# Performance work log

Measured on AMD Instinct MI355X. Metric: run time of the kernel, lower is better.

The kernel has to match this reference:

```python
import jax, jax.numpy as jnp
from jax import lax
import numpy as np

WINDOW = 51
HALF = WINDOW // 2  # 25
K_SAUVOLA = 0.2     # skimage threshold_sauvola default k
RGB_W = np.array([0.2989, 0.5870, 0.1140], dtype=np.float32)  # tf.image.rgb_to_grayscale weights


def _window_sum(x, axis):
    """Sliding-window sum of length WINDOW along `axis`, 'same' size, reflect padding.
    O(1) per pixel via cumulative sums (integral-image style), matching the
    uniform_filter-based local statistics in skimage's Sauvola."""
    pad = [(0, 0)] * x.ndim
    pad[axis] = (HALF, HALF)
    xp = jnp.pad(x, pad, mode='reflect')
    cs = jnp.cumsum(xp, axis=axis)
    zshape = list(cs.shape)
    zshape[axis] = 1
    cs = jnp.concatenate([jnp.zeros(zshape, cs.dtype), cs], axis=axis)
    n = cs.shape[axis]
    hi = lax.slice_in_dim(cs, WINDOW, n, axis=axis)
    lo = lax.slice_in_dim(cs, 0, n - WINDOW, axis=axis)
    return hi - lo


def _box_mean(x):
    # separable 51x51 box filter over H (axis 1) and W (axis 2)
    s = _window_sum(_window_sum(x, axis=1), axis=2)
    return s / jnp.asarray(WINDOW * WINDOW, x.dtype)


def setup_inputs() -> dict:
    key = jax.random.key(0)
    inputs = jax.random.uniform(key, (8, 1024, 1024, 3), dtype=jnp.float32)
    return {"inputs": inputs}


def reference(inputs) -> jnp.ndarray:
    # RGB -> grayscale (channels == 3 branch), keep channel dim [B,H,W,1]
    gray = jnp.einsum('bhwc,c->bhw', inputs, jnp.asarray(RGB_W))[..., None]
    # local mean / std over 51x51 window
    m = _box_mean(gray)
    m2 = _box_mean(gray * gray)
    var = jnp.maximum(m2 - m * m, 0.0)
    s = jnp.sqrt(var)
    # skimage default dynamic range: r = 0.5 * (max - min) over the whole array
    r = 0.5 * (jnp.max(gray) - jnp.min(gray))
    thresh = m * (1.0 + K_SAUVOLA * (s / r - 1.0))
    # (gray > thresh) * 1
    return (gray > thresh).astype(jnp.float32)
```

## Files before the change

### kernel.cpp

```cpp
#include <hip/hip_runtime.h>

#define IMW 1024
#define IMH 1024
#define NB  8
#define HALF 25
#define STRIP 64
#define NCELL 64

#define W_R ((double)0.2989f)
#define W_G ((double)0.5870f)
#define W_B ((double)0.1140f)
#define INV_AREA (1.0 / 2601.0)

__device__ __forceinline__ int refl(int i, int n) {
    if (i < 0) i = -i;
    if (i >= n) i = 2 * n - 2 - i;
    return i;
}

__device__ __forceinline__ double wsum(const double* __restrict__ C, int p) {
    int a = p + HALF; if (a > IMW - 1) a = IMW - 1;
    int b = p - HALF - 1;
    double s = C[a] - (b >= 0 ? C[b] : 0.0);
    if (p <= HALF - 1)      s += C[HALF - p] - C[0];
    if (p >= IMW - HALF)    s += C[IMW - 2] - C[2*IMW - 2 - HALF - 1 - p];
    return s;
}

__global__ void k0_init(unsigned long long* cells) {
    cells[threadIdx.x] = ~0ULL;
    cells[NCELL + threadIdx.x] = 0ULL;
}

__global__ __launch_bounds__(256) void k1_rowpass(const float* __restrict__ in,
                                                  double2* __restrict__ hp,
                                                  unsigned long long* __restrict__ cells) {
    __shared__ double cs1[IMW];
    __shared__ double cs2[IMW];
    __shared__ double wt1[4], wt2[4], bmin[4], bmax[4];
    const int row = blockIdx.x;
    const long long base = (long long)row * IMW;
    const int t = threadIdx.x;
    const int lane = t & 63, w = t >> 6;

    const float4* p4 = (const float4*)(in + base * 3);
    float4 f0 = p4[3*t], f1 = p4[3*t+1], f2 = p4[3*t+2];
    double g0 = (double)f0.x*W_R + (double)f0.y*W_G + (double)f0.z*W_B;
    double g1 = (double)f0.w*W_R + (double)f1.x*W_G + (double)f1.y*W_B;
    double g2 = (double)f1.z*W_R + (double)f1.w*W_G + (double)f2.x*W_B;
    double g3 = (double)f2.y*W_R + (double)f2.z*W_G + (double)f2.w*W_B;

    double l1_0 = g0, l1_1 = l1_0 + g1, l1_2 = l1_1 + g2, l1_3 = l1_2 + g3;
    double q0 = g0*g0, q1 = g1*g1, q2 = g2*g2, q3 = g3*g3;
    double l2_0 = q0, l2_1 = l2_0 + q1, l2_2 = l2_1 + q2, l2_3 = l2_2 + q3;

    double lmin = fmin(fmin(g0, g1), fmin(g2, g3));
    double lmax = fmax(fmax(g0, g1), fmax(g2, g3));
    for (int off = 32; off; off >>= 1) {
        lmin = fmin(lmin, __shfl_down(lmin, off));
        lmax = fmax(lmax, __shfl_down(lmax, off));
    }
    if (lane == 0) { bmin[w] = lmin; bmax[w] = lmax; }

    double v1 = l1_3, v2 = l2_3;
    for (int off = 1; off < 64; off <<= 1) {
        double u1 = __shfl_up(v1, off);
        double u2 = __shfl_up(v2, off);
        if (lane >= off) { v1 += u1; v2 += u2; }
    }
    if (lane == 63) { wt1[w] = v1; wt2[w] = v2; }
    __syncthreads();
    double e1 = v1 - l1_3, e2 = v2 - l2_3;
    for (int j = 0; j < w; j++) { e1 += wt1[j]; e2 += wt2[j]; }

    double2* c1 = (double2*)&cs1[4*t];
    double2* c2 = (double2*)&cs2[4*t];
    c1[0] = make_double2(e1 + l1_0, e1 + l1_1);
    c1[1] = make_double2(e1 + l1_2, e1 + l1_3);
    c2[0] = make_double2(e2 + l2_0, e2 + l2_1);
    c2[1] = make_double2(e2 + l2_2, e2 + l2_3);

    if (t == 0) {
        double m0 = fmin(fmin(bmin[0], bmin[1]), fmin(bmin[2], bmin[3]));
        double m1 = fmax(fmax(bmax[0], bmax[1]), fmax(bmax[2], bmax[3]));
        int cell = row & (NCELL - 1);
        atomicMin(&cells[cell], (unsigned long long)__double_as_longlong(m0));
        atomicMax(&cells[NCELL + cell], (unsigned long long)__double_as_longlong(m1));
    }
    __syncthreads();

    for (int k = 0; k < 4; k++) {
        int p = t + 256 * k;
        hp[base + p] = make_double2(wsum(cs1, p), wsum(cs2, p));
    }
}

__global__ __launch_bounds__(256) void k2_colpass(const float* __restrict__ in,
                                                  const double2* __restrict__ hp,
                                                  const unsigned long long* __restrict__ cells,
                                                  float* __restrict__ out) {
    __shared__ double sr[2];
    const int t = threadIdx.x;
    if (t < 64) {
        unsigned long long mn = cells[t];
        unsigned long long mx = cells[NCELL + t];
        for (int off = 32; off; off >>= 1) {
            unsigned long long a = __shfl_down(mn, off);
            unsigned long long b = __shfl_down(mx, off);
            mn = (a < mn) ? a : mn;
            mx = (b > mx) ? b : mx;
        }
        if (t == 0) {
            sr[0] = __longlong_as_double((long long)mn);
            sr[1] = __longlong_as_double((long long)mx);
        }
    }
    __syncthreads();
    const double r  = 0.5 * (sr[1] - sr[0]);
    const double r2 = r * r;

    const int id   = blockIdx.x;
    const int b    = id & 7;
    const int rest = id >> 3;
    const int ys   = rest & 15;
    const int xc   = rest >> 4;
    const int x  = xc * 256 + t;
    const int y0 = ys * STRIP;
    const long long ib = (long long)b * IMH * IMW;

    double2 v = make_double2(0.0, 0.0);
    #pragma unroll 8
    for (int j = -HALF; j <= HALF; j++) {
        int ry = refl(y0 + j, IMH);
        double2 h = hp[ib + (long long)ry * IMW + x];
        v.x += h.x; v.y += h.y;
    }

    #pragma unroll 8
    for (int y = y0; y < y0 + STRIP; y++) {
        long long pix = ib + (long long)y * IMW + x;
        const float* p = in + pix * 3;
        double g = (double)p[0]*W_R + (double)p[1]*W_G + (double)p[2]*W_B;

        double m  = v.x * INV_AREA;
        double va = fmax(v.y * INV_AREA - m * m, 0.0);
        double A  = g - 0.8 * m;
        int o = (A > 0.0) && (A * A * r2 > 0.04 * m * m * va);
        out[pix] = o ? 1.0f : 0.0f;

        int ra = refl(y + HALF + 1, IMH);
        int rs = refl(y - HALF, IMH);
        double2 ha = hp[ib + (long long)ra * IMW + x];
        double2 hs = hp[ib + (long long)rs * IMW + x];
        v.x += ha.x - hs.x;
        v.y += ha.y - hs.y;
    }
}

extern "C" void kernel_launch(void* const* d_in, const int* in_sizes, int n_in,
                              void* d_out, int out_size, void* d_ws, size_t ws_size,
                              hipStream_t stream) {
    const float* in = (const float*)d_in[0];
    float* out = (float*)d_out;

    unsigned long long* cells = (unsigned long long*)d_ws;
    double2* hp = (double2*)((char*)d_ws + 4096);

    hipLaunchKernelGGL(k0_init, dim3(1), dim3(NCELL), 0, stream, cells);
    hipLaunchKernelGGL(k1_rowpass, dim3(NB * IMH), dim3(256), 0, stream,
                       in, hp, cells);
    hipLaunchKernelGGL(k2_colpass, dim3((IMW / 256) * (IMH / STRIP) * NB), dim3(256), 0, stream,
                       in, hp, cells, out);
}
```

Before: 237.6 us.

## Replace sliding column sum with slab-wise vertical prefix sums plus carry

The row pass now handles 8-row slabs per block and writes running vertical prefix sums of the horizontal window sums within each slab. A new carry kernel computes per-slab column offsets. The column pass then gets each window sum in O(1) from prefix differences, so it no longer needs a 51-row warmup, and it uses shorter strips for more parallelism. In exchange it adds an extra kernel launch and more random-ish hp reads per pixel (about 4 double2 loads instead of 2), and prefix sums in double may lose some precision.

```diff
diff --git a/kernel.cpp b/kernel.cpp
--- a/kernel.cpp
+++ b/kernel.cpp
@@ -4,19 +4,15 @@
 #define IMH 1024
 #define NB  8
 #define HALF 25
-#define STRIP 64
+#define SLAB 8
+#define NSLAB (IMH / SLAB)
+#define STRIP 16
 #define NCELL 64
 
 #define W_R ((double)0.2989f)
 #define W_G ((double)0.5870f)
 #define W_B ((double)0.1140f)
 #define INV_AREA (1.0 / 2601.0)
-
-__device__ __forceinline__ int refl(int i, int n) {
-    if (i < 0) i = -i;
-    if (i >= n) i = 2 * n - 2 - i;
-    return i;
-}
 
 __device__ __forceinline__ double wsum(const double* __restrict__ C, int p) {
     int a = p + HALF; if (a > IMW - 1) a = IMW - 1;
@@ -32,73 +28,106 @@
     cells[NCELL + threadIdx.x] = 0ULL;
 }
 
-__global__ __launch_bounds__(256) void k1_rowpass(const float* __restrict__ in,
-                                                  double2* __restrict__ hp,
-                                                  unsigned long long* __restrict__ cells) {
+__global__ __launch_bounds__(256) void k1_slab(const float* __restrict__ in,
+                                               double2* __restrict__ hp,
+                                               unsigned long long* __restrict__ cells) {
     __shared__ double cs1[IMW];
     __shared__ double cs2[IMW];
-    __shared__ double wt1[4], wt2[4], bmin[4], bmax[4];
-    const int row = blockIdx.x;
-    const long long base = (long long)row * IMW;
+    __shared__ double wt1[4], wt2[4];
+    const int blk = blockIdx.x;
+    const int b = blk / NSLAB;
+    const int s = blk % NSLAB;
+    const int r0 = s * SLAB;
     const int t = threadIdx.x;
     const int lane = t & 63, w = t >> 6;
 
-    const float4* p4 = (const float4*)(in + base * 3);
-    float4 f0 = p4[3*t], f1 = p4[3*t+1], f2 = p4[3*t+2];
-    double g0 = (double)f0.x*W_R + (double)f0.y*W_G + (double)f0.z*W_B;
-    double g1 = (double)f0.w*W_R + (double)f1.x*W_G + (double)f1.y*W_B;
-    double g2 = (double)f1.z*W_R + (double)f1.w*W_G + (double)f2.x*W_B;
-    double g3 = (double)f2.y*W_R + (double)f2.z*W_G + (double)f2.w*W_B;
-
-    double l1_0 = g0, l1_1 = l1_0 + g1, l1_2 = l1_1 + g2, l1_3 = l1_2 + g3;
-    double q0 = g0*g0, q1 = g1*g1, q2 = g2*g2, q3 = g3*g3;
-    double l2_0 = q0, l2_1 = l2_0 + q1, l2_2 = l2_1 + q2, l2_3 = l2_2 + q3;
-
-    double lmin = fmin(fmin(g0, g1), fmin(g2, g3));
-    double lmax = fmax(fmax(g0, g1), fmax(g2, g3));
+    double acc1[4] = {0.0, 0.0, 0.0, 0.0};
+    double acc2[4] = {0.0, 0.0, 0.0, 0.0};
+    double lmin = 1e300, lmax = -1e300;
+
+    for (int r = 0; r < SLAB; r++) {
+        const int row = r0 + r;
+        const long long base = ((long long)b * IMH + row) * IMW;
+
+        const float4* p4 = (const float4*)(in + base * 3);
+        float4 f0 = p4[3*t], f1 = p4[3*t+1], f2 = p4[3*t+2];
+        double g0 = (double)f0.x*W_R + (double)f0.y*W_G + (double)f0.z*W_B;
+        double g1 = (double)f0.w*W_R + (double)f1.x*W_G + (double)f1.y*W_B;
+        double g2 = (double)f1.z*W_R + (double)f1.w*W_G + (double)f2.x*W_B;
+        double g3 = (double)f2.y*W_R + (double)f2.z*W_G + (double)f2.w*W_B;
+
+        double l1_0 = g0, l1_1 = l1_0 + g1, l1_2 = l1_1 + g2, l1_3 = l1_2 + g3;
+        double q0 = g0*g0, q1 = g1*g1, q2 = g2*g2, q3 = g3*g3;
+        double l2_0 = q0, l2_1 = l2_0 + q1, l2_2 = l2_1 + q2, l2_3 = l2_2 + q3;
+
+        lmin = fmin(lmin, fmin(fmin(g0, g1), fmin(g2, g3)));
+        lmax = fmax(lmax, fmax(fmax(g0, g1), fmax(g2, g3)));
+
+        double v1 = l1_3, v2 = l2_3;
+        for (int off = 1; off < 64; off <<= 1) {
+            double u1 = __shfl_up(v1, off);
+            double u2 = __shfl_up(v2, off);
+            if (lane >= off) { v1 += u1; v2 += u2; }
+        }
+        __syncthreads();
+        if (lane == 63) { wt1[w] = v1; wt2[w] = v2; }
+        __syncthreads();
+        double e1 = v1 - l1_3, e2 = v2 - l2_3;
+        for (int j = 0; j < w; j++) { e1 += wt1[j]; e2 += wt2[j]; }
+
+        double2* c1 = (double2*)&cs1[4*t];
+        double2* c2 = (double2*)&cs2[4*t];
+        c1[0] = make_double2(e1 + l1_0, e1 + l1_1);
+        c1[1] = make_double2(e1 + l1_2, e1 + l1_3);
+        c2[0] = make_double2(e2 + l2_0, e2 + l2_1);
+        c2[1] = make_double2(e2 + l2_2, e2 + l2_3);
+        __syncthreads();
+
+        #pragma unroll
+        for (int k = 0; k < 4; k++) {
+            int p = t + 256 * k;
+            acc1[k] += wsum(cs1, p);
+            acc2[k] += wsum(cs2, p);
+            hp[base + p] = make_double2(acc1[k], acc2[k]);
+        }
+    }
+
     for (int off = 32; off; off >>= 1) {
         lmin = fmin(lmin, __shfl_down(lmin, off));
         lmax = fmax(lmax, __shfl_down(lmax, off));
     }
+    __shared__ double bmin[4], bmax[4];
     if (lane == 0) { bmin[w] = lmin; bmax[w] = lmax; }
-
-    double v1 = l1_3, v2 = l2_3;
-    for (int off = 1; off < 64; off <<= 1) {
-        double u1 = __shfl_up(v1, off);
-        double u2 = __shfl_up(v2, off);
-        if (lane >= off) { v1 += u1; v2 += u2; }
-    }
-    if (lane == 63) { wt1[w] = v1; wt2[w] = v2; }
     __syncthreads();
-    double e1 = v1 - l1_3, e2 = v2 - l2_3;
-    for (int j = 0; j < w; j++) { e1 += wt1[j]; e2 += wt2[j]; }
-
-    double2* c1 = (double2*)&cs1[4*t];
-    double2* c2 = (double2*)&cs2[4*t];
-    c1[0] = make_double2(e1 + l1_0, e1 + l1_1);
-    c1[1] = make_double2(e1 + l1_2, e1 + l1_3);
-    c2[0] = make_double2(e2 + l2_0, e2 + l2_1);
-    c2[1] = make_double2(e2 + l2_2, e2 + l2_3);
-
     if (t == 0) {
         double m0 = fmin(fmin(bmin[0], bmin[1]), fmin(bmin[2], bmin[3]));
         double m1 = fmax(fmax(bmax[0], bmax[1]), fmax(bmax[2], bmax[3]));
-        int cell = row & (NCELL - 1);
+        int cell = blk & (NCELL - 1);
         atomicMin(&cells[cell], (unsigned long long)__double_as_longlong(m0));
         atomicMax(&cells[NCELL + cell], (unsigned long long)__double_as_longlong(m1));
     }
-    __syncthreads();
-
-    for (int k = 0; k < 4; k++) {
-        int p = t + 256 * k;
-        hp[base + p] = make_double2(wsum(cs1, p), wsum(cs2, p));
-    }
-}
-
-__global__ __launch_bounds__(256) void k2_colpass(const float* __restrict__ in,
-                                                  const double2* __restrict__ hp,
-                                                  const unsigned long long* __restrict__ cells,
-                                                  float* __restrict__ out) {
+}
+
+__global__ __launch_bounds__(256) void k1c_carry(const double2* __restrict__ hp,
+                                                 double2* __restrict__ carry) {
+    const int tid = blockIdx.x * 256 + threadIdx.x;
+    const int b = tid >> 10;
+    const int col = tid & (IMW - 1);
+    double a1 = 0.0, a2 = 0.0;
+    #pragma unroll 8
+    for (int s = 0; s < NSLAB; s++) {
+        carry[((long long)b * NSLAB + s) * IMW + col] = make_double2(a1, a2);
+        double2 v = hp[((long long)b * IMH + s * SLAB + SLAB - 1) * IMW + col];
+        a1 += v.x;
+        a2 += v.y;
+    }
+}
+
+__global__ __launch_bounds__(256) void k2_cpass(const float* __restrict__ in,
+                                                const double2* __restrict__ hp,
+                                                const double2* __restrict__ carry,
+                                                const unsigned long long* __restrict__ cells,
+                                                float* __restrict__ out) {
     __shared__ double sr[2];
     const int t = threadIdx.x;
     if (t < 64) {
@@ -106,9 +135,9 @@
         unsigned long long mx = cells[NCELL + t];
         for (int off = 32; off; off >>= 1) {
             unsigned long long a = __shfl_down(mn, off);
-            unsigned long long b = __shfl_down(mx, off);
+            unsigned long long b2 = __shfl_down(mx, off);
             mn = (a < mn) ? a : mn;
-            mx = (b > mx) ? b : mx;
+            mx = (b2 > mx) ? b2 : mx;
         }
         if (t == 0) {
             sr[0] = __longlong_as_double((long long)mn);
@@ -122,38 +151,57 @@
     const int id   = blockIdx.x;
     const int b    = id & 7;
     const int rest = id >> 3;
-    const int ys   = rest & 15;
-    const int xc   = rest >> 4;
-    const int x  = xc * 256 + t;
+    const int ys   = rest & 63;
+    const int xt   = rest >> 6;
+    const int x  = xt * 256 + t;
     const int y0 = ys * STRIP;
     const long long ib = (long long)b * IMH * IMW;
-
-    double2 v = make_double2(0.0, 0.0);
-    #pragma unroll 8
-    for (int j = -HALF; j <= HALF; j++) {
-        int ry = refl(y0 + j, IMH);
-        double2 h = hp[ib + (long long)ry * IMW + x];
-        v.x += h.x; v.y += h.y;
-    }
-
-    #pragma unroll 8
+    const double2* Cb = hp + ib;
+    const double2* Kb = carry + (long long)b * NSLAB * IMW;
+
+    #pragma unroll 2
     for (int y = y0; y < y0 + STRIP; y++) {
+        const int top = (y + HALF > IMH - 1) ? (IMH - 1) : (y + HALF);
+        const int bot = y - HALF - 1;
+
+        double2 ct = Cb[(long long)top * IMW + x];
+        double2 kt = Kb[(long long)(top >> 3) * IMW + x];
+        double V1 = ct.x + kt.x;
+        double V2 = ct.y + kt.y;
+        if (bot >= 0) {
+            double2 cbv = Cb[(long long)bot * IMW + x];
+            double2 kbv = Kb[(long long)(bot >> 3) * IMW + x];
+            V1 -= cbv.x + kbv.x;
+            V2 -= cbv.y + kbv.y;
+        }
+        if (y <= HALF - 1) {
+            int ma = HALF - y;
+            double2 c1 = Cb[(long long)ma * IMW + x];
+            double2 k1 = Kb[(long long)(ma >> 3) * IMW + x];
+            double2 c0 = Cb[x];
+            double2 k0 = Kb[x];
+            V1 += (c1.x + k1.x) - (c0.x + k0.x);
+            V2 += (c1.y + k1.y) - (c0.y + k0.y);
+        }
+        if (y + HALF > IMH - 1) {
+            int mz = 2 * IMH - 4 - HALF - y + 1;
+            double2 c1 = Cb[(long long)(IMH - 2) * IMW + x];
+            double2 k1 = Kb[(long long)((IMH - 2) >> 3) * IMW + x];
+            double2 c0 = Cb[(long long)mz * IMW + x];
+            double2 k0 = Kb[(long long)(mz >> 3) * IMW + x];
+            V1 += (c1.x + k1.x) - (c0.x + k0.x);
+            V2 += (c1.y + k1.y) - (c0.y + k0.y);
+        }
+
         long long pix = ib + (long long)y * IMW + x;
         const float* p = in + pix * 3;
         double g = (double)p[0]*W_R + (double)p[1]*W_G + (double)p[2]*W_B;
 
-        double m  = v.x * INV_AREA;
-        double va = fmax(v.y * INV_AREA - m * m, 0.0);
+        double m  = V1 * INV_AREA;
+        double va = fmax(V2 * INV_AREA - m * m, 0.0);
         double A  = g - 0.8 * m;
         int o = (A > 0.0) && (A * A * r2 > 0.04 * m * m * va);
         out[pix] = o ? 1.0f : 0.0f;
-
-        int ra = refl(y + HALF + 1, IMH);
-        int rs = refl(y - HALF, IMH);
-        double2 ha = hp[ib + (long long)ra * IMW + x];
-        double2 hs = hp[ib + (long long)rs * IMW + x];
-        v.x += ha.x - hs.x;
-        v.y += ha.y - hs.y;
     }
 }
 
@@ -165,10 +213,13 @@
 
     unsigned long long* cells = (unsigned long long*)d_ws;
     double2* hp = (double2*)((char*)d_ws + 4096);
+    double2* carry = hp + (size_t)NB * IMH * IMW;
 
     hipLaunchKernelGGL(k0_init, dim3(1), dim3(NCELL), 0, stream, cells);
-    hipLaunchKernelGGL(k1_rowpass, dim3(NB * IMH), dim3(256), 0, stream,
+    hipLaunchKernelGGL(k1_slab, dim3(NB * NSLAB), dim3(256), 0, stream,
                        in, hp, cells);
-    hipLaunchKernelGGL(k2_colpass, dim3((IMW / 256) * (IMH / STRIP) * NB), dim3(256), 0, stream,
-                       in, hp, cells, out);
-}
+    hipLaunchKernelGGL(k1c_carry, dim3(NB * IMW / 256), dim3(256), 0, stream,
+                       hp, carry);
+    hipLaunchKernelGGL(k2_cpass, dim3((IMW / 256) * (IMH / STRIP) * NB), dim3(256), 0, stream,
+                       in, hp, carry, cells, out);
+}
```

After: 272.2 us. +14.6%, slower.

## Add per-slab column partial sums to shortcut column-window initialization

Applied to the files above, without the earlier changes.

The row pass now processes 8-row slabs per block and, besides the horizontal window sums, writes per-slab column sums of those values. The column pass initializes its 51-row vertical window from these slab sums plus a few edge rows instead of reading all 51 rows, and it skips the unused final slide. This reduces global reads in the column pass, at the cost of an extra workspace buffer and fewer, longer row-pass blocks with more barriers.

```diff
diff --git a/kernel.cpp b/kernel.cpp
--- a/kernel.cpp
+++ b/kernel.cpp
@@ -4,7 +4,10 @@
 #define IMH 1024
 #define NB  8
 #define HALF 25
+#define SLAB 8
+#define NSLAB (IMH / SLAB)
 #define STRIP 64
+#define NSTRIP (IMH / STRIP)
 #define NCELL 64
 
 #define W_R ((double)0.2989f)
@@ -32,71 +35,117 @@
     cells[NCELL + threadIdx.x] = 0ULL;
 }
 
-__global__ __launch_bounds__(256) void k1_rowpass(const float* __restrict__ in,
-                                                  double2* __restrict__ hp,
-                                                  unsigned long long* __restrict__ cells) {
+__global__ __launch_bounds__(256) void k1_slab(const float* __restrict__ in,
+                                               double2* __restrict__ hp,
+                                               double2* __restrict__ Sv,
+                                               unsigned long long* __restrict__ cells) {
     __shared__ double cs1[IMW];
     __shared__ double cs2[IMW];
-    __shared__ double wt1[4], wt2[4], bmin[4], bmax[4];
-    const int row = blockIdx.x;
-    const long long base = (long long)row * IMW;
+    __shared__ double wt1[4], wt2[4];
+    const int blk = blockIdx.x;
+    const int b = blk / NSLAB;
+    const int s = blk % NSLAB;
+    const int r0 = s * SLAB;
     const int t = threadIdx.x;
     const int lane = t & 63, w = t >> 6;
 
-    const float4* p4 = (const float4*)(in + base * 3);
-    float4 f0 = p4[3*t], f1 = p4[3*t+1], f2 = p4[3*t+2];
-    double g0 = (double)f0.x*W_R + (double)f0.y*W_G + (double)f0.z*W_B;
-    double g1 = (double)f0.w*W_R + (double)f1.x*W_G + (double)f1.y*W_B;
-    double g2 = (double)f1.z*W_R + (double)f1.w*W_G + (double)f2.x*W_B;
-    double g3 = (double)f2.y*W_R + (double)f2.z*W_G + (double)f2.w*W_B;
-
-    double l1_0 = g0, l1_1 = l1_0 + g1, l1_2 = l1_1 + g2, l1_3 = l1_2 + g3;
-    double q0 = g0*g0, q1 = g1*g1, q2 = g2*g2, q3 = g3*g3;
-    double l2_0 = q0, l2_1 = l2_0 + q1, l2_2 = l2_1 + q2, l2_3 = l2_2 + q3;
-
-    double lmin = fmin(fmin(g0, g1), fmin(g2, g3));
-    double lmax = fmax(fmax(g0, g1), fmax(g2, g3));
+    double s1[4] = {0.0, 0.0, 0.0, 0.0};
+    double s2[4] = {0.0, 0.0, 0.0, 0.0};
+    double lmin = 1e300, lmax = -1e300;
+
+    for (int r = 0; r < SLAB; r++) {
+        const int row = r0 + r;
+        const long long base = ((long long)b * IMH + row) * IMW;
+
+        const float4* p4 = (const float4*)(in + base * 3);
+        float4 f0 = p4[3*t], f1 = p4[3*t+1], f2 = p4[3*t+2];
+        double g0 = (double)f0.x*W_R + (double)f0.y*W_G + (double)f0.z*W_B;
+        double g1 = (double)f0.w*W_R + (double)f1.x*W_G + (double)f1.y*W_B;
+        double g2 = (double)f1.z*W_R + (double)f1.w*W_G + (double)f2.x*W_B;
+        double g3 = (double)f2.y*W_R + (double)f2.z*W_G + (double)f2.w*W_B;
+
+        double l1_0 = g0, l1_1 = l1_0 + g1, l1_2 = l1_1 + g2, l1_3 = l1_2 + g3;
+        double q0 = g0*g0, q1 = g1*g1, q2 = g2*g2, q3 = g3*g3;
+        double l2_0 = q0, l2_1 = l2_0 + q1, l2_2 = l2_1 + q2, l2_3 = l2_2 + q3;
+
+        lmin = fmin(lmin, fmin(fmin(g0, g1), fmin(g2, g3)));
+        lmax = fmax(lmax, fmax(fmax(g0, g1), fmax(g2, g3)));
+
+        double v1 = l1_3, v2 = l2_3;
+        for (int off = 1; off < 64; off <<= 1) {
+            double u1 = __shfl_up(v1, off);
+            double u2 = __shfl_up(v2, off);
+            if (lane >= off) { v1 += u1; v2 += u2; }
+        }
+        __syncthreads();
+        if (lane == 63) { wt1[w] = v1; wt2[w] = v2; }
+        __syncthreads();
+        double e1 = v1 - l1_3, e2 = v2 - l2_3;
+        for (int j = 0; j < w; j++) { e1 += wt1[j]; e2 += wt2[j]; }
+
+        double2* c1 = (double2*)&cs1[4*t];
+        double2* c2 = (double2*)&cs2[4*t];
+        c1[0] = make_double2(e1 + l1_0, e1 + l1_1);
+        c1[1] = make_double2(e1 + l1_2, e1 + l1_3);
+        c2[0] = make_double2(e2 + l2_0, e2 + l2_1);
+        c2[1] = make_double2(e2 + l2_2, e2 + l2_3);
+        __syncthreads();
+
+        #pragma unroll
+        for (int k = 0; k < 4; k++) {
+            int p = t + 256 * k;
+            double h1 = wsum(cs1, p);
+            double h2 = wsum(cs2, p);
+            hp[base + p] = make_double2(h1, h2);
+            s1[k] += h1;
+            s2[k] += h2;
+        }
+    }
+
+    #pragma unroll
+    for (int k = 0; k < 4; k++) {
+        int p = t + 256 * k;
+        Sv[((long long)b * NSLAB + s) * IMW + p] = make_double2(s1[k], s2[k]);
+    }
+
     for (int off = 32; off; off >>= 1) {
         lmin = fmin(lmin, __shfl_down(lmin, off));
         lmax = fmax(lmax, __shfl_down(lmax, off));
     }
+    __shared__ double bmin[4], bmax[4];
     if (lane == 0) { bmin[w] = lmin; bmax[w] = lmax; }
-
-    double v1 = l1_3, v2 = l2_3;
-    for (int off = 1; off < 64; off <<= 1) {
-        double u1 = __shfl_up(v1, off);
-        double u2 = __shfl_up(v2, off);
-        if (lane >= off) { v1 += u1; v2 += u2; }
-    }
-    if (lane == 63) { wt1[w] = v1; wt2[w] = v2; }
     __syncthreads();
-    double e1 = v1 - l1_3, e2 = v2 - l2_3;
-    for (int j = 0; j < w; j++) { e1 += wt1[j]; e2 += wt2[j]; }
-
-    double2* c1 = (double2*)&cs1[4*t];
-    double2* c2 = (double2*)&cs2[4*t];
-    c1[0] = make_double2(e1 + l1_0, e1 + l1_1);
-    c1[1] = make_double2(e1 + l1_2, e1 + l1_3);
-    c2[0] = make_double2(e2 + l2_0, e2 + l2_1);
-    c2[1] = make_double2(e2 + l2_2, e2 + l2_3);
-
     if (t == 0) {
         double m0 = fmin(fmin(bmin[0], bmin[1]), fmin(bmin[2], bmin[3]));
         double m1 = fmax(fmax(bmax[0], bmax[1]), fmax(bmax[2], bmax[3]));
-        int cell = row & (NCELL - 1);
+        int cell = blk & (NCELL - 1);
         atomicMin(&cells[cell], (unsigned long long)__double_as_longlong(m0));
         atomicMax(&cells[NCELL + cell], (unsigned long long)__double_as_longlong(m1));
     }
-    __syncthreads();
-
-    for (int k = 0; k < 4; k++) {
-        int p = t + 256 * k;
-        hp[base + p] = make_double2(wsum(cs1, p), wsum(cs2, p));
+}
+
+__device__ __forceinline__ void sum_rows(const double2* __restrict__ Hb,
+                                         const double2* __restrict__ Svb,
+                                         int a, int b, int x,
+                                         double& V1, double& V2) {
+    int r = a;
+    while ((r & 7) && r <= b) {
+        double2 h = Hb[(long long)r * IMW + x];
+        V1 += h.x; V2 += h.y; r++;
+    }
+    while (r + 7 <= b) {
+        double2 s = Svb[(long long)(r >> 3) * IMW + x];
+        V1 += s.x; V2 += s.y; r += 8;
+    }
+    while (r <= b) {
+        double2 h = Hb[(long long)r * IMW + x];
+        V1 += h.x; V2 += h.y; r++;
     }
 }
 
 __global__ __launch_bounds__(256) void k2_colpass(const float* __restrict__ in,
                                                   const double2* __restrict__ hp,
+                                                  const double2* __restrict__ Sv,
                                                   const unsigned long long* __restrict__ cells,
                                                   float* __restrict__ out) {
     __shared__ double sr[2];
@@ -106,9 +155,9 @@
         unsigned long long mx = cells[NCELL + t];
         for (int off = 32; off; off >>= 1) {
             unsigned long long a = __shfl_down(mn, off);
-            unsigned long long b = __shfl_down(mx, off);
+            unsigned long long b2 = __shfl_down(mx, off);
             mn = (a < mn) ? a : mn;
-            mx = (b > mx) ? b : mx;
+            mx = (b2 > mx) ? b2 : mx;
         }
         if (t == 0) {
             sr[0] = __longlong_as_double((long long)mn);
@@ -122,19 +171,18 @@
     const int id   = blockIdx.x;
     const int b    = id & 7;
     const int rest = id >> 3;
-    const int ys   = rest & 15;
-    const int xc   = rest >> 4;
-    const int x  = xc * 256 + t;
+    const int ys   = rest & (NSTRIP - 1);
+    const int xt   = rest >> 4;
+    const int x  = xt * 256 + t;
     const int y0 = ys * STRIP;
     const long long ib = (long long)b * IMH * IMW;
-
-    double2 v = make_double2(0.0, 0.0);
-    #pragma unroll 8
-    for (int j = -HALF; j <= HALF; j++) {
-        int ry = refl(y0 + j, IMH);
-        double2 h = hp[ib + (long long)ry * IMW + x];
-        v.x += h.x; v.y += h.y;
-    }
+    const double2* Hb  = hp + ib;
+    const double2* Svb = Sv + (long long)b * NSLAB * IMW;
+
+    double V1 = 0.0, V2 = 0.0;
+    const int lo = y0 - HALF, hi = y0 + HALF;
+    sum_rows(Hb, Svb, lo < 0 ? 0 : lo, hi, x, V1, V2);
+    if (lo < 0) sum_rows(Hb, Svb, 1, -lo, x, V1, V2);
 
     #pragma unroll 8
     for (int y = y0; y < y0 + STRIP; y++) {
@@ -142,18 +190,20 @@
         const float* p = in + pix * 3;
         double g = (double)p[0]*W_R + (double)p[1]*W_G + (double)p[2]*W_B;
 
-        double m  = v.x * INV_AREA;
-        double va = fmax(v.y * INV_AREA - m * m, 0.0);
+        double m  = V1 * INV_AREA;
+        double va = fmax(V2 * INV_AREA - m * m, 0.0);
         double A  = g - 0.8 * m;
         int o = (A > 0.0) && (A * A * r2 > 0.04 * m * m * va);
         out[pix] = o ? 1.0f : 0.0f;
 
-        int ra = refl(y + HALF + 1, IMH);
-        int rs = refl(y - HALF, IMH);
-        double2 ha = hp[ib + (long long)ra * IMW + x];
-        double2 hs = hp[ib + (long long)rs * IMW + x];
-        v.x += ha.x - hs.x;
-        v.y += ha.y - hs.y;
+        if (y + 1 < y0 + STRIP) {
+            int ra = refl(y + HALF + 1, IMH);
+            int rs = refl(y - HALF, IMH);
+            double2 ha = Hb[(long long)ra * IMW + x];
+            double2 hs = Hb[(long long)rs * IMW + x];
+            V1 += ha.x - hs.x;
+            V2 += ha.y - hs.y;
+        }
     }
 }
 
@@ -165,10 +215,11 @@
 
     unsigned long long* cells = (unsigned long long*)d_ws;
     double2* hp = (double2*)((char*)d_ws + 4096);
+    double2* Sv = hp + (size_t)NB * IMH * IMW;
 
     hipLaunchKernelGGL(k0_init, dim3(1), dim3(NCELL), 0, stream, cells);
-    hipLaunchKernelGGL(k1_rowpass, dim3(NB * IMH), dim3(256), 0, stream,
-                       in, hp, cells);
-    hipLaunchKernelGGL(k2_colpass, dim3((IMW / 256) * (IMH / STRIP) * NB), dim3(256), 0, stream,
-                       in, hp, cells, out);
-}
+    hipLaunchKernelGGL(k1_slab, dim3(NB * NSLAB), dim3(256), 0, stream,
+                       in, hp, Sv, cells);
+    hipLaunchKernelGGL(k2_colpass, dim3((IMW / 256) * NSTRIP * NB), dim3(256), 0, stream,
+                       in, hp, Sv, cells, out);
+}
```

After: 262.2 us. 1.1x slower.
